# Kernel optimization log

Measured on AMD Instinct MI355X. Metric: run time of the kernel, lower is better.

## Reference

```python
import jax, jax.numpy as jnp
import numpy as np

D_MODEL = 1024


def setup_inputs() -> dict:
    key = jax.random.key(0)
    k_x, k_qkv, k_proj, k_b = jax.random.split(key, 4)
    b, t, d = 4, 2048, D_MODEL
    scale = 1.0 / np.sqrt(d)
    x = jax.random.normal(k_x, (b, t, d), dtype=jnp.float32)
    # torch Linear(d, 3d, bias=False): weight [3d, d]; we store transposed [d, 3d]
    w_qkv = jax.random.normal(k_qkv, (d, 3 * d), dtype=jnp.float32) * scale
    w_proj = jax.random.normal(k_proj, (d, d), dtype=jnp.float32) * scale
    b_proj = jax.random.normal(k_b, (d,), dtype=jnp.float32) * scale
    return {"x": x, "w_qkv": w_qkv, "w_proj": w_proj, "b_proj": b_proj}


def reference(x, w_qkv, w_proj, b_proj):
    b, t, d = x.shape
    qkv = jnp.einsum("btd,de->bte", x, w_qkv)  # [b, t, 3d]
    q, k, v = jnp.split(qkv, 3, axis=-1)
    att = jnp.einsum("btd,bsd->bts", q, k) / jnp.sqrt(jnp.float32(d))  # [b, t, t]
    causal = jnp.tril(jnp.ones((t, t), dtype=bool))
    att = jnp.where(causal, att, -jnp.inf)
    att = jax.nn.softmax(att, axis=-1)
    out = jnp.einsum("bts,bsd->btd", att, v)
    return jnp.einsum("btd,de->bte", out, w_proj) + b_proj
```

## Files before the change

### kernel.cpp

```cpp
#include <hip/hip_runtime.h>


typedef __bf16 bf16x8_t __attribute__((ext_vector_type(8)));
typedef float  f32x16_t __attribute__((ext_vector_type(16)));
typedef unsigned short u16;

struct alignas(8) u16x4 { u16 x, y, z, w; };

__device__ inline float bf2f(u16 u) {
  union { unsigned u; float f; } c; c.u = ((unsigned)u) << 16; return c.f;
}
__device__ inline u16 f2bf(float f) {
  union { float f; unsigned u; } c; c.f = f;
  unsigned r = c.u + 0x7fffu + ((c.u >> 16) & 1u);
  return (u16)(r >> 16);
}

template<int OUTMODE, int GRIDMODE>
__global__ __launch_bounds__(256, 4)
void gemm_bt(const u16* __restrict__ A, const u16* __restrict__ B,
             void* __restrict__ Cv, u16* __restrict__ C2,
             const float* __restrict__ bias, float* __restrict__ rs,
             int K, int lda, int ldb, int ldc,
             long sA, long sB, long sC)
{
  int bn0, bm0;
  if (GRIDMODE == 1) {
    const int x = blockIdx.x;
    int r = (int)((sqrtf(8.f * x + 1.f) - 1.f) * 0.5f);
    while ((r + 1) * (r + 2) / 2 <= x) ++r;
    while (r * (r + 1) / 2 > x) --r;
    bm0 = r * 128;
    bn0 = (x - r * (r + 1) / 2) * 128;
  } else if (GRIDMODE == 2) {
    bn0 = blockIdx.x * 128;
    bm0 = ((int)gridDim.y - 1 - (int)blockIdx.y) * 128;
  } else {
    bn0 = blockIdx.x * 128;
    bm0 = blockIdx.y * 128;
  }
  const long bz = blockIdx.z;
  const u16* Ab = A + bz * sA;
  const u16* Bb = B + bz * sB;
  const int Keff = (GRIDMODE == 2) ? min(K, bm0 + 128) : K;

  __shared__ __align__(16) u16 lA[128 * 64];
  __shared__ __align__(16) u16 lB[128 * 64];

  const int tid  = threadIdx.x;
  const int lane = tid & 63;
  const int wv   = tid >> 6;
  const int wm   = (wv >> 1) << 6;
  const int wn   = (wv & 1) << 6;
  const int ml   = lane & 31;
  const int kh   = lane >> 5;
  const int swz  = ml & 7;

  f32x16_t acc[2][2];
#pragma unroll
  for (int i = 0; i < 2; ++i)
#pragma unroll
    for (int j = 0; j < 2; ++j)
#pragma unroll
      for (int r = 0; r < 16; ++r)
        acc[i][j][r] = 0.f;

  const long ldA2 = (long)lda * 2, ldB2 = (long)ldb * 2;
  const int rowA = tid >> 3;
  const int csw  = (tid & 7) ^ (rowA & 7);
  const char* pA = (const char*)(Ab + (long)bm0 * lda) + (long)rowA * ldA2 + (csw << 4);
  const char* pB = (const char*)(Bb + (long)bn0 * ldb) + (long)rowA * ldB2 + (csw << 4);
  const int ldsbo = tid * 16;

  for (int k0 = 0; k0 < Keff; k0 += 64) {
    const long kb = (long)k0 * 2;
#pragma unroll
    for (int r = 0; r < 4; ++r)
      __builtin_amdgcn_global_load_lds(
          (const __attribute__((address_space(1))) unsigned int*)(pA + kb + (long)(r * 32) * ldA2),
          (__attribute__((address_space(3))) unsigned int*)((char*)lA + ldsbo + r * 4096), 16, 0, 0);
#pragma unroll
    for (int r = 0; r < 4; ++r)
      __builtin_amdgcn_global_load_lds(
          (const __attribute__((address_space(1))) unsigned int*)(pB + kb + (long)(r * 32) * ldB2),
          (__attribute__((address_space(3))) unsigned int*)((char*)lB + ldsbo + r * 4096), 16, 0, 0);
    __syncthreads();

#pragma unroll
    for (int s = 0; s < 4; ++s) {
      const int ck = ((s * 2 + kh) ^ swz) << 3;
      bf16x8_t a0 = *(const bf16x8_t*)&lA[(wm + ml) * 64 + ck];
      bf16x8_t a1 = *(const bf16x8_t*)&lA[(wm + 32 + ml) * 64 + ck];
      bf16x8_t b0 = *(const bf16x8_t*)&lB[(wn + ml) * 64 + ck];
      bf16x8_t b1 = *(const bf16x8_t*)&lB[(wn + 32 + ml) * 64 + ck];
      acc[0][0] = __builtin_amdgcn_mfma_f32_32x32x16_bf16(a0, b0, acc[0][0], 0, 0, 0);
      acc[0][1] = __builtin_amdgcn_mfma_f32_32x32x16_bf16(a0, b1, acc[0][1], 0, 0, 0);
      acc[1][0] = __builtin_amdgcn_mfma_f32_32x32x16_bf16(a1, b0, acc[1][0], 0, 0, 0);
      acc[1][1] = __builtin_amdgcn_mfma_f32_32x32x16_bf16(a1, b1, acc[1][1], 0, 0, 0);
    }
    __syncthreads();
  }

  if (OUTMODE == 2) {
    if (bn0 >= 2048) {
#pragma unroll
      for (int i = 0; i < 2; ++i) {
#pragma unroll
        for (int g = 0; g < 4; ++g) {
          const int rowb = bm0 + wm + i * 32 + g * 8 + kh * 4;
          const int b_  = rowb >> 11;
          const int s_  = rowb & 2047;
#pragma unroll
          for (int j = 0; j < 2; ++j) {
            const int dcol = bn0 - 2048 + wn + j * 32 + ml;
            u16x4 o = {f2bf(acc[i][j][g * 4 + 0]), f2bf(acc[i][j][g * 4 + 1]),
                       f2bf(acc[i][j][g * 4 + 2]), f2bf(acc[i][j][g * 4 + 3])};
            *(u16x4*)&C2[(((long)b_ * 1024 + dcol) << 11) + s_] = o;
          }
        }
      }
    } else {
      u16* Cb16 = (u16*)Cv;
#pragma unroll
      for (int i = 0; i < 2; ++i)
#pragma unroll
        for (int j = 0; j < 2; ++j)
#pragma unroll
          for (int reg = 0; reg < 16; ++reg) {
            const int row = bm0 + wm + i * 32 + (reg & 3) + 8 * (reg >> 2) + kh * 4;
            const int col = bn0 + wn + j * 32 + ml;
            Cb16[(long)row * ldc + col] = f2bf(acc[i][j][reg]);
          }
    }
    return;
  }

  if (OUTMODE == 3) {
    const float scale = 0.03125f;
    const bool diag = (bm0 == bn0);
    u16* Cb16 = (u16*)Cv + bz * sC;
    float* rsb = rs + bz * 2048;
#pragma unroll
    for (int i = 0; i < 2; ++i) {
#pragma unroll
      for (int reg = 0; reg < 16; ++reg) {
        const int grow = bm0 + wm + i * 32 + (reg & 3) + 8 * (reg >> 2) + kh * 4;
        const int col0 = bn0 + wn + ml;
        float e0 = (diag && col0 > grow)      ? 0.f : __expf(acc[i][0][reg] * scale);
        float e1 = (diag && col0 + 32 > grow) ? 0.f : __expf(acc[i][1][reg] * scale);
        Cb16[(long)grow * ldc + col0]      = f2bf(e0);
        Cb16[(long)grow * ldc + col0 + 32] = f2bf(e1);
        float rsum = e0 + e1;
#pragma unroll
        for (int m = 1; m < 32; m <<= 1) rsum += __shfl_xor(rsum, m);
        if (ml == 0) atomicAdd(&rsb[grow], rsum);
      }
    }
    return;
  }

  if (OUTMODE == 4) {
    float* rsl = (float*)lA;
    if (tid < 128) rsl[tid] = 1.0f / rs[bz * 2048 + bm0 + tid];
    __syncthreads();
    u16* Cb16 = (u16*)Cv + bz * sC;
#pragma unroll
    for (int i = 0; i < 2; ++i)
#pragma unroll
      for (int j = 0; j < 2; ++j)
#pragma unroll
        for (int reg = 0; reg < 16; ++reg) {
          const int rl  = wm + i * 32 + (reg & 3) + 8 * (reg >> 2) + kh * 4;
          const int col = bn0 + wn + j * 32 + ml;
          Cb16[(long)(bm0 + rl) * ldc + col] = f2bf(acc[i][j][reg] * rsl[rl]);
        }
    return;
  }

  float* Cf32 = (float*)Cv + bz * sC;
#pragma unroll
  for (int i = 0; i < 2; ++i)
#pragma unroll
    for (int j = 0; j < 2; ++j)
#pragma unroll
      for (int reg = 0; reg < 16; ++reg) {
        const int row = bm0 + wm + i * 32 + (reg & 3) + 8 * (reg >> 2) + kh * 4;
        const int col = bn0 + wn + j * 32 + ml;
        Cf32[(long)row * ldc + col] = acc[i][j][reg] + bias[col];
      }
}

__global__ __launch_bounds__(256)
void cvt_f32_bf16(const float* __restrict__ in, u16* __restrict__ out) {
  const int i = blockIdx.x * 256 + threadIdx.x;
  float4 v = ((const float4*)in)[i];
  u16x4 o = {f2bf(v.x), f2bf(v.y), f2bf(v.z), f2bf(v.w)};
  ((u16x4*)out)[i] = o;
}

__global__ __launch_bounds__(256)
void transpose_weights(const float* __restrict__ wqkv, u16* __restrict__ wqkvT,
                       const float* __restrict__ wproj, u16* __restrict__ wprojT) {
  const bool isq = blockIdx.x < 96;
  const float* in = isq ? wqkv : wproj;
  u16* out        = isq ? wqkvT : wprojT;
  const int C     = isq ? 3072 : 1024;
  const int c0 = (isq ? blockIdx.x : (blockIdx.x - 96)) * 32;
  const int r0 = blockIdx.y * 32;
  __shared__ float t[32][33];
  const int tx = threadIdx.x & 31, ty = threadIdx.x >> 5;
#pragma unroll
  for (int i = 0; i < 32; i += 8)
    t[ty + i][tx] = in[(long)(r0 + ty + i) * C + (c0 + tx)];
  __syncthreads();
#pragma unroll
  for (int i = 0; i < 32; i += 8)
    out[(long)(c0 + ty + i) * 1024 + (r0 + tx)] = f2bf(t[tx][ty + i]);
}

extern "C" void kernel_launch(void* const* d_in, const int* in_sizes, int n_in,
                              void* d_out, int out_size, void* d_ws, size_t ws_size,
                              hipStream_t stream) {
  (void)in_sizes; (void)n_in; (void)out_size; (void)ws_size;
  const float* x      = (const float*)d_in[0];
  const float* w_qkv  = (const float*)d_in[1];
  const float* w_proj = (const float*)d_in[2];
  const float* b_proj = (const float*)d_in[3];
  float* y = (float*)d_out;
  char*  ws = (char*)d_ws;

  u16* xbf    = (u16*)(ws);
  u16* qk     = (u16*)(ws + (16l << 20));
  u16* wqkvT  = (u16*)(ws + (48l << 20));
  u16* wprojT = (u16*)(ws + (54l << 20));
  u16* vT     = (u16*)(ws + (56l << 20));
  u16* E      = (u16*)(ws + (72l << 20));
  float* rsum = (float*)(ws + (104l << 20));
  u16* attn   = xbf;

  hipMemsetAsync(rsum, 0, 4 * 2048 * sizeof(float), stream);
  cvt_f32_bf16<<<8192, 256, 0, stream>>>(x, xbf);
  transpose_weights<<<dim3(128, 32), 256, 0, stream>>>(w_qkv, wqkvT, w_proj, wprojT);
  gemm_bt<2, 0><<<dim3(24, 64, 1), 256, 0, stream>>>(
      xbf, wqkvT, qk, vT, nullptr, nullptr, 1024, 1024, 1024, 2048, 0, 0, 0);
  gemm_bt<3, 1><<<dim3(136, 1, 4), 256, 0, stream>>>(
      qk, qk + 1024, E, nullptr, nullptr, rsum, 1024, 2048, 2048, 2048,
      (long)2048 * 2048, (long)2048 * 2048, (long)2048 * 2048);
  gemm_bt<4, 2><<<dim3(8, 16, 4), 256, 0, stream>>>(
      E, vT, attn, nullptr, nullptr, rsum, 2048, 2048, 2048, 1024,
      (long)2048 * 2048, (long)1024 * 2048, (long)2048 * 1024);
  gemm_bt<1, 0><<<dim3(8, 64, 1), 256, 0, stream>>>(
      attn, wprojT, y, nullptr, b_proj, nullptr, 1024, 1024, 1024, 1024, 0, 0, 0);
}
```

Measured before the change: 278.8 us.

## Add 256x256 eight-wave pipelined GEMM for QKV and output projections

Adds a new gemm8p kernel with 256x256 tiles, 8 waves, 16x16x32 MFMAs, double-buffered LDS staging through global_load_lds, explicit barrier/waitcnt scheduling, setprio around MFMA bursts, and an XCD-aware block swizzle. It replaces the old 128x128 kernel for the QKV projection and the output projection. The goal is more data reuse per tile and overlap of loads with compute. In exchange it uses 128KB of LDS, which limits occupancy. With 384 and 128 blocks, the output projection in particular may underfill the GPU.

```diff
diff --git a/kernel.cpp b/kernel.cpp
--- a/kernel.cpp
+++ b/kernel.cpp
@@ -2,6 +2,7 @@
 
 
 typedef __bf16 bf16x8_t __attribute__((ext_vector_type(8)));
+typedef float  f32x4_t  __attribute__((ext_vector_type(4)));
 typedef float  f32x16_t __attribute__((ext_vector_type(16)));
 typedef unsigned short u16;
 
@@ -14,6 +15,187 @@
   union { float f; unsigned u; } c; c.f = f;
   unsigned r = c.u + 0x7fffu + ((c.u >> 16) & 1u);
   return (u16)(r >> 16);
+}
+
+
+#define BAR __builtin_amdgcn_s_barrier()
+#define SCB __builtin_amdgcn_sched_barrier(0)
+#define LGK asm volatile("s_waitcnt lgkmcnt(0)" ::: "memory")
+
+#define STG(pst, base_, ld2, t_, ksh_)                                         \
+  { const char* s0_ = (pst) + ((t_) * 64 + (ksh_) * 32) * 2;                   \
+    char* d0_ = (base_) + (((t_) & 1) << 15) + ((ksh_) << 14) + ldst;          \
+    __builtin_amdgcn_global_load_lds(                                          \
+        (const __attribute__((address_space(1))) unsigned int*)s0_,            \
+        (__attribute__((address_space(3))) unsigned int*)d0_, 16, 0, 0);       \
+    __builtin_amdgcn_global_load_lds(                                          \
+        (const __attribute__((address_space(1))) unsigned int*)(s0_ + 128 * (ld2)), \
+        (__attribute__((address_space(3))) unsigned int*)(d0_ + 8192), 16, 0, 0); }
+
+#define RD_A(lAb, ks, mh)                                                      \
+  a0 = *(const bf16x8_t*)((lAb) + (ks) * 16384 + (mh) * 4096 + 0 * 1024);      \
+  a1 = *(const bf16x8_t*)((lAb) + (ks) * 16384 + (mh) * 4096 + 1 * 1024);      \
+  a2 = *(const bf16x8_t*)((lAb) + (ks) * 16384 + (mh) * 4096 + 2 * 1024);      \
+  a3 = *(const bf16x8_t*)((lAb) + (ks) * 16384 + (mh) * 4096 + 3 * 1024);
+
+#define RD_B(lBb, ks)                                                          \
+  b0 = *(const bf16x8_t*)((lBb) + (ks) * 16384 + 0 * 1024);                    \
+  b1 = *(const bf16x8_t*)((lBb) + (ks) * 16384 + 1 * 1024);                    \
+  b2 = *(const bf16x8_t*)((lBb) + (ks) * 16384 + 2 * 1024);                    \
+  b3 = *(const bf16x8_t*)((lBb) + (ks) * 16384 + 3 * 1024);
+
+#define MM(mh)                                                                 \
+  acc[(mh)*4+0][0] = __builtin_amdgcn_mfma_f32_16x16x32_bf16(a0, b0, acc[(mh)*4+0][0], 0, 0, 0); \
+  acc[(mh)*4+0][1] = __builtin_amdgcn_mfma_f32_16x16x32_bf16(a0, b1, acc[(mh)*4+0][1], 0, 0, 0); \
+  acc[(mh)*4+0][2] = __builtin_amdgcn_mfma_f32_16x16x32_bf16(a0, b2, acc[(mh)*4+0][2], 0, 0, 0); \
+  acc[(mh)*4+0][3] = __builtin_amdgcn_mfma_f32_16x16x32_bf16(a0, b3, acc[(mh)*4+0][3], 0, 0, 0); \
+  acc[(mh)*4+1][0] = __builtin_amdgcn_mfma_f32_16x16x32_bf16(a1, b0, acc[(mh)*4+1][0], 0, 0, 0); \
+  acc[(mh)*4+1][1] = __builtin_amdgcn_mfma_f32_16x16x32_bf16(a1, b1, acc[(mh)*4+1][1], 0, 0, 0); \
+  acc[(mh)*4+1][2] = __builtin_amdgcn_mfma_f32_16x16x32_bf16(a1, b2, acc[(mh)*4+1][2], 0, 0, 0); \
+  acc[(mh)*4+1][3] = __builtin_amdgcn_mfma_f32_16x16x32_bf16(a1, b3, acc[(mh)*4+1][3], 0, 0, 0); \
+  acc[(mh)*4+2][0] = __builtin_amdgcn_mfma_f32_16x16x32_bf16(a2, b0, acc[(mh)*4+2][0], 0, 0, 0); \
+  acc[(mh)*4+2][1] = __builtin_amdgcn_mfma_f32_16x16x32_bf16(a2, b1, acc[(mh)*4+2][1], 0, 0, 0); \
+  acc[(mh)*4+2][2] = __builtin_amdgcn_mfma_f32_16x16x32_bf16(a2, b2, acc[(mh)*4+2][2], 0, 0, 0); \
+  acc[(mh)*4+2][3] = __builtin_amdgcn_mfma_f32_16x16x32_bf16(a2, b3, acc[(mh)*4+2][3], 0, 0, 0); \
+  acc[(mh)*4+3][0] = __builtin_amdgcn_mfma_f32_16x16x32_bf16(a3, b0, acc[(mh)*4+3][0], 0, 0, 0); \
+  acc[(mh)*4+3][1] = __builtin_amdgcn_mfma_f32_16x16x32_bf16(a3, b1, acc[(mh)*4+3][1], 0, 0, 0); \
+  acc[(mh)*4+3][2] = __builtin_amdgcn_mfma_f32_16x16x32_bf16(a3, b2, acc[(mh)*4+3][2], 0, 0, 0); \
+  acc[(mh)*4+3][3] = __builtin_amdgcn_mfma_f32_16x16x32_bf16(a3, b3, acc[(mh)*4+3][3], 0, 0, 0);
+
+template<int OUTMODE>
+__global__ __launch_bounds__(512, 2)
+void gemm8p(const u16* __restrict__ A, const u16* __restrict__ B,
+            void* __restrict__ Cv, u16* __restrict__ C2,
+            const float* __restrict__ bias,
+            int K, int lda, int ldb, int ldc)
+{
+  const int nx  = gridDim.x;
+  const int nwg = nx * gridDim.y;
+  const int lin = blockIdx.y * nx + blockIdx.x;
+  const int cpx = nwg >> 3;
+  const int swz = (lin & 7) * cpx + (lin >> 3);
+  const int bn0 = (swz % nx) * 256;
+  const int bm0 = (swz / nx) * 256;
+
+  __shared__ __align__(16) u16 lds[65536];
+  char* const baseA = (char*)lds;
+  char* const baseB = (char*)lds + 65536;
+
+  const int tid  = threadIdx.x;
+  const int lane = tid & 63;
+  const int wv   = tid >> 6;
+  const int wrow = ((wv >> 2) & 1) * 128;
+  const int wcol = (wv & 3) * 64;
+  const int l15  = lane & 15;
+  const int rd_pl = l15 * 64 + ((((lane >> 4) ^ (l15 >> 1)) & 3) << 4);
+
+  const int c_src = (tid & 3) ^ ((tid >> 3) & 3);
+  const int s_row = tid >> 2;
+  const int ldst  = tid * 16;
+  const long ldA2 = (long)lda * 2, ldB2 = (long)ldb * 2;
+  const char* pAst = (const char*)A + ((long)bm0 + s_row) * ldA2 + c_src * 16;
+  const char* pBst = (const char*)B + ((long)bn0 + s_row) * ldB2 + c_src * 16;
+
+  f32x4_t acc[8][4];
+#pragma unroll
+  for (int i = 0; i < 8; ++i)
+#pragma unroll
+    for (int j = 0; j < 4; ++j)
+      acc[i][j] = (f32x4_t){0.f, 0.f, 0.f, 0.f};
+
+  const int nt = K >> 6;
+
+  STG(pAst, baseA, ldA2, 0, 0);
+  STG(pBst, baseB, ldB2, 0, 0);
+  STG(pAst, baseA, ldA2, 0, 1);
+  STG(pBst, baseB, ldB2, 0, 1);
+  if (nt > 1) STG(pAst, baseA, ldA2, 1, 0);
+  asm volatile("s_waitcnt vmcnt(6)" ::: "memory");
+  BAR; SCB;
+
+  bf16x8_t a0, a1, a2, a3, b0, b1, b2, b3;
+
+  for (int t = 0; t < nt; ++t) {
+    const char* lAb = baseA + ((t & 1) << 15) + wrow * 64 + rd_pl;
+    const char* lBb = baseB + ((t & 1) << 15) + wcol * 64 + rd_pl;
+    const bool st1 = (t + 1 < nt), st2 = (t + 2 < nt);
+
+    RD_B(lBb, 0);
+    RD_A(lAb, 0, 0);
+    if (st1) STG(pBst, baseB, ldB2, t + 1, 0);
+    BAR; LGK; SCB;
+    __builtin_amdgcn_s_setprio(1); MM(0); __builtin_amdgcn_s_setprio(0);
+    BAR; SCB;
+
+    RD_A(lAb, 0, 1);
+    if (st1) STG(pAst, baseA, ldA2, t + 1, 1);
+    BAR; LGK; SCB;
+    __builtin_amdgcn_s_setprio(1); MM(1); __builtin_amdgcn_s_setprio(0);
+    if (st1) { asm volatile("s_waitcnt vmcnt(6)" ::: "memory"); }
+    else     { asm volatile("s_waitcnt vmcnt(0)" ::: "memory"); }
+    BAR; SCB;
+
+    RD_B(lBb, 1);
+    RD_A(lAb, 1, 0);
+    if (st1) STG(pBst, baseB, ldB2, t + 1, 1);
+    BAR; LGK; SCB;
+    __builtin_amdgcn_s_setprio(1); MM(0); __builtin_amdgcn_s_setprio(0);
+    BAR; SCB;
+
+    RD_A(lAb, 1, 1);
+    if (st2) STG(pAst, baseA, ldA2, t + 2, 0);
+    BAR; LGK; SCB;
+    __builtin_amdgcn_s_setprio(1); MM(1); __builtin_amdgcn_s_setprio(0);
+    if (st1) {
+      if (st2) { asm volatile("s_waitcnt vmcnt(6)" ::: "memory"); }
+      else     { asm volatile("s_waitcnt vmcnt(4)" ::: "memory"); }
+    }
+    BAR; SCB;
+  }
+
+  const int rb = bm0 + wrow + ((lane >> 4) << 2);
+
+  if (OUTMODE == 2) {
+    if (bn0 >= 2048) {
+#pragma unroll
+      for (int mi = 0; mi < 8; ++mi) {
+        const int s0 = rb + mi * 16;
+        const int b_ = s0 >> 11;
+        const int s_ = s0 & 2047;
+#pragma unroll
+        for (int ni = 0; ni < 4; ++ni) {
+          const int dcol = bn0 - 2048 + wcol + ni * 16 + l15;
+          u16x4 o = {f2bf(acc[mi][ni][0]), f2bf(acc[mi][ni][1]),
+                     f2bf(acc[mi][ni][2]), f2bf(acc[mi][ni][3])};
+          *(u16x4*)&C2[(((long)b_ * 1024 + dcol) << 11) + s_] = o;
+        }
+      }
+    } else {
+      u16* Cb16 = (u16*)Cv;
+#pragma unroll
+      for (int mi = 0; mi < 8; ++mi)
+#pragma unroll
+        for (int ni = 0; ni < 4; ++ni) {
+          const int col = bn0 + wcol + ni * 16 + l15;
+#pragma unroll
+          for (int r = 0; r < 4; ++r)
+            Cb16[(long)(rb + mi * 16 + r) * ldc + col] = f2bf(acc[mi][ni][r]);
+        }
+    }
+    return;
+  }
+
+  float* Cf32 = (float*)Cv;
+#pragma unroll
+  for (int mi = 0; mi < 8; ++mi)
+#pragma unroll
+    for (int ni = 0; ni < 4; ++ni) {
+      const int col = bn0 + wcol + ni * 16 + l15;
+      const float bb = bias[col];
+#pragma unroll
+      for (int r = 0; r < 4; ++r)
+        Cf32[(long)(rb + mi * 16 + r) * ldc + col] = acc[mi][ni][r] + bb;
+    }
 }
 
 template<int OUTMODE, int GRIDMODE>
@@ -54,7 +236,7 @@
   const int wn   = (wv & 1) << 6;
   const int ml   = lane & 31;
   const int kh   = lane >> 5;
-  const int swz  = ml & 7;
+  const int swzl = ml & 7;
 
   f32x16_t acc[2][2];
 #pragma unroll
@@ -88,51 +270,17 @@
 
 #pragma unroll
     for (int s = 0; s < 4; ++s) {
-      const int ck = ((s * 2 + kh) ^ swz) << 3;
-      bf16x8_t a0 = *(const bf16x8_t*)&lA[(wm + ml) * 64 + ck];
-      bf16x8_t a1 = *(const bf16x8_t*)&lA[(wm + 32 + ml) * 64 + ck];
-      bf16x8_t b0 = *(const bf16x8_t*)&lB[(wn + ml) * 64 + ck];
-      bf16x8_t b1 = *(const bf16x8_t*)&lB[(wn + 32 + ml) * 64 + ck];
-      acc[0][0] = __builtin_amdgcn_mfma_f32_32x32x16_bf16(a0, b0, acc[0][0], 0, 0, 0);
-      acc[0][1] = __builtin_amdgcn_mfma_f32_32x32x16_bf16(a0, b1, acc[0][1], 0, 0, 0);
-      acc[1][0] = __builtin_amdgcn_mfma_f32_32x32x16_bf16(a1, b0, acc[1][0], 0, 0, 0);
-      acc[1][1] = __builtin_amdgcn_mfma_f32_32x32x16_bf16(a1, b1, acc[1][1], 0, 0, 0);
+      const int ck = ((s * 2 + kh) ^ swzl) << 3;
+      bf16x8_t A0 = *(const bf16x8_t*)&lA[(wm + ml) * 64 + ck];
+      bf16x8_t A1 = *(const bf16x8_t*)&lA[(wm + 32 + ml) * 64 + ck];
+      bf16x8_t B0 = *(const bf16x8_t*)&lB[(wn + ml) * 64 + ck];
+      bf16x8_t B1 = *(const bf16x8_t*)&lB[(wn + 32 + ml) * 64 + ck];
+      acc[0][0] = __builtin_amdgcn_mfma_f32_32x32x16_bf16(A0, B0, acc[0][0], 0, 0, 0);
+      acc[0][1] = __builtin_amdgcn_mfma_f32_32x32x16_bf16(A0, B1, acc[0][1], 0, 0, 0);
+      acc[1][0] = __builtin_amdgcn_mfma_f32_32x32x16_bf16(A1, B0, acc[1][0], 0, 0, 0);
+      acc[1][1] = __builtin_amdgcn_mfma_f32_32x32x16_bf16(A1, B1, acc[1][1], 0, 0, 0);
     }
     __syncthreads();
-  }
-
-  if (OUTMODE == 2) {
-    if (bn0 >= 2048) {
-#pragma unroll
-      for (int i = 0; i < 2; ++i) {
-#pragma unroll
-        for (int g = 0; g < 4; ++g) {
-          const int rowb = bm0 + wm + i * 32 + g * 8 + kh * 4;
-          const int b_  = rowb >> 11;
-          const int s_  = rowb & 2047;
-#pragma unroll
-          for (int j = 0; j < 2; ++j) {
-            const int dcol = bn0 - 2048 + wn + j * 32 + ml;
-            u16x4 o = {f2bf(acc[i][j][g * 4 + 0]), f2bf(acc[i][j][g * 4 + 1]),
-                       f2bf(acc[i][j][g * 4 + 2]), f2bf(acc[i][j][g * 4 + 3])};
-            *(u16x4*)&C2[(((long)b_ * 1024 + dcol) << 11) + s_] = o;
-          }
-        }
-      }
-    } else {
-      u16* Cb16 = (u16*)Cv;
-#pragma unroll
-      for (int i = 0; i < 2; ++i)
-#pragma unroll
-        for (int j = 0; j < 2; ++j)
-#pragma unroll
-          for (int reg = 0; reg < 16; ++reg) {
-            const int row = bm0 + wm + i * 32 + (reg & 3) + 8 * (reg >> 2) + kh * 4;
-            const int col = bn0 + wn + j * 32 + ml;
-            Cb16[(long)row * ldc + col] = f2bf(acc[i][j][reg]);
-          }
-    }
-    return;
   }
 
   if (OUTMODE == 3) {
@@ -176,18 +324,6 @@
         }
     return;
   }
-
-  float* Cf32 = (float*)Cv + bz * sC;
-#pragma unroll
-  for (int i = 0; i < 2; ++i)
-#pragma unroll
-    for (int j = 0; j < 2; ++j)
-#pragma unroll
-      for (int reg = 0; reg < 16; ++reg) {
-        const int row = bm0 + wm + i * 32 + (reg & 3) + 8 * (reg >> 2) + kh * 4;
-        const int col = bn0 + wn + j * 32 + ml;
-        Cf32[(long)row * ldc + col] = acc[i][j][reg] + bias[col];
-      }
 }
 
 __global__ __launch_bounds__(256)
@@ -241,14 +377,14 @@
   hipMemsetAsync(rsum, 0, 4 * 2048 * sizeof(float), stream);
   cvt_f32_bf16<<<8192, 256, 0, stream>>>(x, xbf);
   transpose_weights<<<dim3(128, 32), 256, 0, stream>>>(w_qkv, wqkvT, w_proj, wprojT);
-  gemm_bt<2, 0><<<dim3(24, 64, 1), 256, 0, stream>>>(
-      xbf, wqkvT, qk, vT, nullptr, nullptr, 1024, 1024, 1024, 2048, 0, 0, 0);
+  gemm8p<2><<<dim3(12, 32), 512, 0, stream>>>(
+      xbf, wqkvT, qk, vT, nullptr, 1024, 1024, 1024, 2048);
   gemm_bt<3, 1><<<dim3(136, 1, 4), 256, 0, stream>>>(
       qk, qk + 1024, E, nullptr, nullptr, rsum, 1024, 2048, 2048, 2048,
       (long)2048 * 2048, (long)2048 * 2048, (long)2048 * 2048);
   gemm_bt<4, 2><<<dim3(8, 16, 4), 256, 0, stream>>>(
       E, vT, attn, nullptr, nullptr, rsum, 2048, 2048, 2048, 1024,
       (long)2048 * 2048, (long)1024 * 2048, (long)2048 * 1024);
-  gemm_bt<1, 0><<<dim3(8, 64, 1), 256, 0, stream>>>(
-      attn, wprojT, y, nullptr, b_proj, nullptr, 1024, 1024, 1024, 1024, 0, 0, 0);
-}
+  gemm8p<1><<<dim3(4, 32), 512, 0, stream>>>(
+      attn, wprojT, y, nullptr, b_proj, 1024, 1024, 1024, 1024);
+}
```

New measurement: 285.4 us. 2.4% more time.

## Compute softmax row sums inside PV GEMM instead of atomics in score kernel

Applied to the files above, without the earlier changes.

Removes the warp-shuffle reductions and global atomicAdd of row sums from the exp/score kernel and the memset that zeroed them. The PV GEMM instead sums each row of the E tile already staged in LDS during every k-step and normalises with the local total. This trades atomic traffic and a memset launch for extra LDS reads and adds that are repeated by every column block.

```diff
diff --git a/kernel.cpp b/kernel.cpp
--- a/kernel.cpp
+++ b/kernel.cpp
@@ -20,7 +20,7 @@
 __global__ __launch_bounds__(256, 4)
 void gemm_bt(const u16* __restrict__ A, const u16* __restrict__ B,
              void* __restrict__ Cv, u16* __restrict__ C2,
-             const float* __restrict__ bias, float* __restrict__ rs,
+             const float* __restrict__ bias,
              int K, int lda, int ldb, int ldc,
              long sA, long sB, long sC)
 {
@@ -65,6 +65,8 @@
       for (int r = 0; r < 16; ++r)
         acc[i][j][r] = 0.f;
 
+  float rsacc = 0.f;
+
   const long ldA2 = (long)lda * 2, ldB2 = (long)ldb * 2;
   const int rowA = tid >> 3;
   const int csw  = (tid & 7) ^ (rowA & 7);
@@ -98,6 +100,18 @@
       acc[1][0] = __builtin_amdgcn_mfma_f32_32x32x16_bf16(a1, b0, acc[1][0], 0, 0, 0);
       acc[1][1] = __builtin_amdgcn_mfma_f32_32x32x16_bf16(a1, b1, acc[1][1], 0, 0, 0);
     }
+
+    if (OUTMODE == 4) {
+      const int rr = tid >> 1;
+      const int hh = (tid & 1) << 2;
+#pragma unroll
+      for (int c = 0; c < 4; ++c) {
+        const int cc = hh + ((c + rr) & 3);
+        bf16x8_t v = *(const bf16x8_t*)&lA[rr * 64 + cc * 8];
+#pragma unroll
+        for (int e = 0; e < 8; ++e) rsacc += (float)v[e];
+      }
+    }
     __syncthreads();
   }
 
@@ -139,7 +153,6 @@
     const float scale = 0.03125f;
     const bool diag = (bm0 == bn0);
     u16* Cb16 = (u16*)Cv + bz * sC;
-    float* rsb = rs + bz * 2048;
 #pragma unroll
     for (int i = 0; i < 2; ++i) {
 #pragma unroll
@@ -150,10 +163,6 @@
         float e1 = (diag && col0 + 32 > grow) ? 0.f : __expf(acc[i][1][reg] * scale);
         Cb16[(long)grow * ldc + col0]      = f2bf(e0);
         Cb16[(long)grow * ldc + col0 + 32] = f2bf(e1);
-        float rsum = e0 + e1;
-#pragma unroll
-        for (int m = 1; m < 32; m <<= 1) rsum += __shfl_xor(rsum, m);
-        if (ml == 0) atomicAdd(&rsb[grow], rsum);
       }
     }
     return;
@@ -161,7 +170,10 @@
 
   if (OUTMODE == 4) {
     float* rsl = (float*)lA;
-    if (tid < 128) rsl[tid] = 1.0f / rs[bz * 2048 + bm0 + tid];
+    rsl[tid] = rsacc;
+    __syncthreads();
+    float* rinv = (float*)lB;
+    if (tid < 128) rinv[tid] = 1.0f / (rsl[2 * tid] + rsl[2 * tid + 1]);
     __syncthreads();
     u16* Cb16 = (u16*)Cv + bz * sC;
 #pragma unroll
@@ -172,7 +184,7 @@
         for (int reg = 0; reg < 16; ++reg) {
           const int rl  = wm + i * 32 + (reg & 3) + 8 * (reg >> 2) + kh * 4;
           const int col = bn0 + wn + j * 32 + ml;
-          Cb16[(long)(bm0 + rl) * ldc + col] = f2bf(acc[i][j][reg] * rsl[rl]);
+          Cb16[(long)(bm0 + rl) * ldc + col] = f2bf(acc[i][j][reg] * rinv[rl]);
         }
     return;
   }
@@ -235,20 +247,18 @@
   u16* wprojT = (u16*)(ws + (54l << 20));
   u16* vT     = (u16*)(ws + (56l << 20));
   u16* E      = (u16*)(ws + (72l << 20));
-  float* rsum = (float*)(ws + (104l << 20));
   u16* attn   = xbf;
 
-  hipMemsetAsync(rsum, 0, 4 * 2048 * sizeof(float), stream);
   cvt_f32_bf16<<<8192, 256, 0, stream>>>(x, xbf);
   transpose_weights<<<dim3(128, 32), 256, 0, stream>>>(w_qkv, wqkvT, w_proj, wprojT);
   gemm_bt<2, 0><<<dim3(24, 64, 1), 256, 0, stream>>>(
-      xbf, wqkvT, qk, vT, nullptr, nullptr, 1024, 1024, 1024, 2048, 0, 0, 0);
+      xbf, wqkvT, qk, vT, nullptr, 1024, 1024, 1024, 2048, 0, 0, 0);
   gemm_bt<3, 1><<<dim3(136, 1, 4), 256, 0, stream>>>(
-      qk, qk + 1024, E, nullptr, nullptr, rsum, 1024, 2048, 2048, 2048,
+      qk, qk + 1024, E, nullptr, nullptr, 1024, 2048, 2048, 2048,
       (long)2048 * 2048, (long)2048 * 2048, (long)2048 * 2048);
   gemm_bt<4, 2><<<dim3(8, 16, 4), 256, 0, stream>>>(
-      E, vT, attn, nullptr, nullptr, rsum, 2048, 2048, 2048, 1024,
+      E, vT, attn, nullptr, nullptr, 2048, 2048, 2048, 1024,
       (long)2048 * 2048, (long)1024 * 2048, (long)2048 * 1024);
   gemm_bt<1, 0><<<dim3(8, 64, 1), 256, 0, stream>>>(
-      attn, wprojT, y, nullptr, b_proj, nullptr, 1024, 1024, 1024, 1024, 0, 0, 0);
-}
+      attn, wprojT, y, nullptr, b_proj, 1024, 1024, 1024, 1024, 0, 0, 0);
+}
```

Measured after the change: 274.3 us. About the same (-1.6%).
